# Kernel tuning notes

Hardware: AMD Instinct MI355X
Metric: run time of the kernel (lower is better)

## Reference

```python
import jax, jax.numpy as jnp
import numpy as np

TEMPERATURE = 0.2
EPS = 1e-12


def setup_inputs() -> dict:
    key = jax.random.key(0)
    k1, k2 = jax.random.split(key)
    x = jax.random.normal(k1, (16384, 2048), dtype=jnp.float32)
    protos = jax.random.normal(k2, (4096, 2048), dtype=jnp.float32)
    # buffer is initialized as row-normalized in the torch module
    protos = protos / jnp.maximum(jnp.linalg.norm(protos, axis=1, keepdims=True), EPS)
    return {"x": x, "prototypes": protos, "k": 16}


def reference(x, prototypes, k):
    # L2-normalize inputs (torch F.normalize uses eps clamp on the norm)
    xn = x / jnp.maximum(jnp.linalg.norm(x, axis=-1, keepdims=True), EPS)
    # cosine similarities: (B, P)
    sims = jnp.einsum("bd,pd->bp", xn, prototypes)
    topk_vals, topk_idx = jax.lax.top_k(sims, k)          # (B, k)
    topk_softmax = jax.nn.softmax(topk_vals / TEMPERATURE, axis=-1)
    rows = jnp.arange(sims.shape[0])[:, None]             # (B, 1)
    sparse_act = jnp.zeros_like(sims).at[rows, topk_idx].set(topk_softmax)
    return sparse_act
```

## Files before the change

### kernel.cpp

```cpp
#include <hip/hip_runtime.h>
#include <hip/hip_bf16.h>
#include <stdint.h>

typedef __attribute__((ext_vector_type(8))) short bf16x8;
typedef __attribute__((ext_vector_type(4))) float f32x4;
typedef unsigned short u16;

#define M_ROWS 16384
#define N_COLS 4096
#define K_DIM  2048
#define TOPK   16
#define KSEL   16
#define CAP    48
#define INV_T  5.0f
#define DELTA  0.05f

#define BM 128
#define BN 128
#define BK 64
#define NKT (K_DIM / BK)

__device__ __forceinline__ void async_cp16(const void* g, void* l) {
  __builtin_amdgcn_global_load_lds((const __attribute__((address_space(1))) uint32_t*)g,
                                   (__attribute__((address_space(3))) uint32_t*)l,
                                   16, 0, 0);
}

__device__ __forceinline__ u16 f2bf(float f) {
  __hip_bfloat16 h = __float2bfloat16(f);
  return *reinterpret_cast<u16*>(&h);
}
__device__ __forceinline__ float bf2f(u16 u) {
  return __uint_as_float(((uint32_t)u) << 16);
}
__device__ __forceinline__ uint2 pack4(float4 v) {
  uint2 r;
  r.x = (uint32_t)f2bf(v.x) | ((uint32_t)f2bf(v.y) << 16);
  r.y = (uint32_t)f2bf(v.z) | ((uint32_t)f2bf(v.w) << 16);
  return r;
}

__global__ __launch_bounds__(256) void prep_x_kernel(
    const float* __restrict__ x, u16* __restrict__ xh, float* __restrict__ invn) {
  const int row = blockIdx.x;
  const int t = threadIdx.x;
  const float4* xr = reinterpret_cast<const float4*>(x + (size_t)row * K_DIM);
  float4 v0 = xr[t];
  float4 v1 = xr[256 + t];
  float s = v0.x*v0.x + v0.y*v0.y + v0.z*v0.z + v0.w*v0.w
          + v1.x*v1.x + v1.y*v1.y + v1.z*v1.z + v1.w*v1.w;
  #pragma unroll
  for (int off = 1; off < 64; off <<= 1) s += __shfl_xor(s, off);
  __shared__ float ws4[4];
  if ((t & 63) == 0) ws4[t >> 6] = s;
  __syncthreads();
  if (t == 0) {
    float tot = ws4[0] + ws4[1] + ws4[2] + ws4[3];
    invn[row] = 1.0f / fmaxf(sqrtf(tot), 1e-12f);
  }
  uint2* xo = reinterpret_cast<uint2*>(xh + (size_t)row * K_DIM);
  xo[t] = pack4(v0);
  xo[256 + t] = pack4(v1);
}

__global__ __launch_bounds__(256) void prep_p_kernel(
    const float* __restrict__ p, u16* __restrict__ ph) {
  const int row = blockIdx.x;
  const int t = threadIdx.x;
  const float4* pr = reinterpret_cast<const float4*>(p + (size_t)row * K_DIM);
  uint2* po = reinterpret_cast<uint2*>(ph + (size_t)row * K_DIM);
  po[t] = pack4(pr[t]);
  po[256 + t] = pack4(pr[256 + t]);
}

__global__ __launch_bounds__(256) void gemm_bf16_kernel(
    const u16* __restrict__ A, const u16* __restrict__ B, u16* __restrict__ C) {
  __shared__ __align__(16) u16 sA[2][BM * BK];
  __shared__ __align__(16) u16 sB[2][BN * BK];
  const int t = threadIdx.x;
  const int lane = t & 63;
  const int wid = t >> 6;
  const int wm = wid >> 1, wn = wid & 1;
  const int tm0 = blockIdx.y * BM;
  const int tn0 = blockIdx.x * BN;
  const int lr = lane & 15;
  const int hi = lane >> 4;

  f32x4 acc[4][4];
  #pragma unroll
  for (int i = 0; i < 4; ++i)
    #pragma unroll
    for (int j = 0; j < 4; ++j)
      acc[i][j] = (f32x4){0.f, 0.f, 0.f, 0.f};

  int srow[4], soff[4];
  #pragma unroll
  for (int i = 0; i < 4; ++i) {
    int c = i * 256 + t;
    int r = c >> 3;
    int ib = (c & 7) << 4;
    srow[i] = r;
    soff[i] = ib ^ ((r & 7) << 4);
  }
  const char* Abase = (const char*)(A + (size_t)tm0 * K_DIM);
  const char* Bbase = (const char*)(B + (size_t)tn0 * K_DIM);

#define STAGE(slot, kt_) do {                                                 \
    const int kb_ = (kt_) * (BK * 2);                                         \
    _Pragma("unroll")                                                         \
    for (int i = 0; i < 4; ++i) {                                             \
      async_cp16(Abase + (size_t)srow[i] * (K_DIM * 2) + kb_ + soff[i],       \
                 (char*)sA[slot] + (i * 256 + t) * 16);                       \
      async_cp16(Bbase + (size_t)srow[i] * (K_DIM * 2) + kb_ + soff[i],       \
                 (char*)sB[slot] + (i * 256 + t) * 16);                       \
    }                                                                         \
  } while (0)

  STAGE(0, 0);
  STAGE(1, 1);

  for (int kt = 0; kt < NKT; ++kt) {
    if (kt + 1 < NKT) asm volatile("s_waitcnt vmcnt(8)" ::: "memory");
    else              asm volatile("s_waitcnt vmcnt(0)" ::: "memory");
    __builtin_amdgcn_sched_barrier(0);
    __builtin_amdgcn_s_barrier();
    asm volatile("" ::: "memory");

    const char* cA = (const char*)sA[kt & 1];
    const char* cB = (const char*)sB[kt & 1];
    bf16x8 af[4][2], bq[4][2];
    #pragma unroll
    for (int f = 0; f < 4; ++f) {
      #pragma unroll
      for (int kk = 0; kk < 2; ++kk) {
        int rowA = wm * 64 + f * 16 + lr;
        int inbA = (kk * 64 + (hi << 4)) ^ ((rowA & 7) << 4);
        af[f][kk] = *reinterpret_cast<const bf16x8*>(cA + rowA * 128 + inbA);
        int rowB = wn * 64 + f * 16 + lr;
        int inbB = (kk * 64 + (hi << 4)) ^ ((rowB & 7) << 4);
        bq[f][kk] = *reinterpret_cast<const bf16x8*>(cB + rowB * 128 + inbB);
      }
    }
    asm volatile("s_waitcnt lgkmcnt(0)" ::: "memory");
    __builtin_amdgcn_sched_barrier(0);
    if (kt + 2 < NKT) {
      __builtin_amdgcn_s_barrier();
      asm volatile("" ::: "memory");
      __builtin_amdgcn_sched_barrier(0);
      STAGE(kt & 1, kt + 2);
    }
    __builtin_amdgcn_s_setprio(1);
    #pragma unroll
    for (int kk = 0; kk < 2; ++kk)
      #pragma unroll
      for (int i = 0; i < 4; ++i)
        #pragma unroll
        for (int j = 0; j < 4; ++j)
          acc[i][j] = __builtin_amdgcn_mfma_f32_16x16x32_bf16(
              af[i][kk], bq[j][kk], acc[i][j], 0, 0, 0);
    __builtin_amdgcn_s_setprio(0);
  }
#undef STAGE

  #pragma unroll
  for (int i = 0; i < 4; ++i) {
    #pragma unroll
    for (int j = 0; j < 4; ++j) {
      int colg = tn0 + wn * 64 + j * 16 + lr;
      int rowb = tm0 + wm * 64 + i * 16 + (hi << 2);
      #pragma unroll
      for (int r = 0; r < 4; ++r) {
        __builtin_nontemporal_store(f2bf(acc[i][j][r]),
                                    &C[(size_t)(rowb + r) * N_COLS + colg]);
      }
    }
  }
}

__global__ __launch_bounds__(256) void topk_kernel(
    const float* __restrict__ x, const float* __restrict__ protos,
    const float* __restrict__ invn, const u16* __restrict__ sims,
    int* __restrict__ sposg, float* __restrict__ svalg) {
  const int row = blockIdx.x;
  const int t = threadIdx.x;
  const int lane = t & 63;
  const int wid = t >> 6;

  __shared__ __align__(16) f32x4 lx[512];
  __shared__ int hist[4][257];
  __shared__ int selInfo[2];
  __shared__ int   wtotC[4], wtotW[4];
  __shared__ int   cposC[16];
  __shared__ float cargC[16];
  __shared__ int   wpos[CAP];
  __shared__ float cexact[CAP];
  __shared__ int   spos[TOPK];
  __shared__ float sval[TOPK];

  const bf16x8* orow8 = reinterpret_cast<const bf16x8*>(sims + (size_t)row * N_COLS);
  float fv[16];
  uint32_t key[16];
  #pragma unroll
  for (int i = 0; i < 2; ++i) {
    bf16x8 v = __builtin_nontemporal_load(orow8 + i * 256 + t);
    #pragma unroll
    for (int c = 0; c < 8; ++c) {
      u16 u = (u16)v[c];
      fv[i * 8 + c] = bf2f(u);
      key[i * 8 + c] = (u & 0x8000) ? (uint32_t)(~u & 0xFFFF)
                                    : (uint32_t)(u | 0x8000);
    }
  }

  const f32x4* xr = reinterpret_cast<const f32x4*>(x + (size_t)row * K_DIM);
  lx[t] = __builtin_nontemporal_load(xr + t);
  lx[256 + t] = __builtin_nontemporal_load(xr + 256 + t);

  uint32_t T = 0;
  int K_rem = KSEL;
  #pragma unroll
  for (int pass = 0; pass < 2; ++pass) {
    const int shift = 8 - pass * 8;
    hist[0][t] = 0; hist[1][t] = 0; hist[2][t] = 0; hist[3][t] = 0;
    __syncthreads();
    #pragma unroll
    for (int j = 0; j < 16; ++j) {
      bool ok = (pass == 0) || ((key[j] >> 8) == T);
      if (ok) atomicAdd(&hist[wid][(key[j] >> shift) & 255], 1);
    }
    __syncthreads();
    if (wid == 0) {
      const int b0 = lane << 2;
      int h0 = hist[0][b0]     + hist[1][b0]     + hist[2][b0]     + hist[3][b0];
      int h1 = hist[0][b0 + 1] + hist[1][b0 + 1] + hist[2][b0 + 1] + hist[3][b0 + 1];
      int h2 = hist[0][b0 + 2] + hist[1][b0 + 2] + hist[2][b0 + 2] + hist[3][b0 + 2];
      int h3 = hist[0][b0 + 3] + hist[1][b0 + 3] + hist[2][b0 + 3] + hist[3][b0 + 3];
      int loc = h0 + h1 + h2 + h3;
      int s = loc;
      #pragma unroll
      for (int off = 1; off < 64; off <<= 1) {
        int o = __shfl_down(s, off);
        if (lane + off < 64) s += o;
      }
      const int tail = s - loc;
      int s3 = tail + h3;
      int s2 = s3 + h2;
      int s1 = s2 + h1;
      int s0 = s1 + h0;
      int ge[4] = {s0, s1, s2, s3};
      int hh[4] = {h0, h1, h2, h3};
      #pragma unroll
      for (int k = 0; k < 4; ++k) {
        int gt = ge[k] - hh[k];
        if (gt < K_rem && ge[k] >= K_rem) {
          selInfo[0] = b0 + k;
          selInfo[1] = K_rem - gt;
        }
      }
    }
    __syncthreads();
    T = (T << 8) | (uint32_t)selInfo[0];
    K_rem = selInfo[1];
  }
  const u16 ub = (T & 0x8000) ? (u16)(T ^ 0x8000) : (u16)(~T & 0xFFFF);
  const float a16 = bf2f(ub);
  const float vhi = a16 + DELTA;
  const float vlo = a16 - DELTA;
  const float inv = invn[row];

  int lcC = 0, lcW = 0;
  #pragma unroll
  for (int j = 0; j < 16; ++j) {
    float v = fv[j];
    if (v > vhi) ++lcC;
    else if (v >= vlo) ++lcW;
  }
  int pC = lcC, pW = lcW;
  #pragma unroll
  for (int off = 1; off < 64; off <<= 1) {
    int oC = __shfl_up(pC, off);
    int oW = __shfl_up(pW, off);
    if (lane >= off) { pC += oC; pW += oW; }
  }
  if (lane == 63) { wtotC[wid] = pC; wtotW[wid] = pW; }
  __syncthreads();
  int baseC = pC - lcC, baseW = pW - lcW;
  for (int w2 = 0; w2 < wid; ++w2) { baseC += wtotC[w2]; baseW += wtotW[w2]; }
  const int m  = wtotC[0] + wtotC[1] + wtotC[2] + wtotC[3];
  const int wc = min(wtotW[0] + wtotW[1] + wtotW[2] + wtotW[3], CAP);
  #pragma unroll
  for (int j = 0; j < 16; ++j) {
    float v = fv[j];
    int pos = (j >> 3) * 2048 + t * 8 + (j & 7);
    if (v > vhi) { cposC[baseC] = pos; cargC[baseC] = v; ++baseC; }
    else if (v >= vlo) { if (baseW < CAP) { wpos[baseW] = pos; ++baseW; } }
  }
  __syncthreads();

  for (int ci = wid; ci < wc; ci += 4) {
    int pidx = wpos[ci];
    const f32x4* pr = reinterpret_cast<const f32x4*>(protos + (size_t)pidx * K_DIM);
    float s = 0.f;
    #pragma unroll
    for (int i = 0; i < 8; ++i) {
      f32x4 pv = pr[i * 64 + lane];
      f32x4 xv = lx[i * 64 + lane];
      s = fmaf(pv.x, xv.x, s);
      s = fmaf(pv.y, xv.y, s);
      s = fmaf(pv.z, xv.z, s);
      s = fmaf(pv.w, xv.w, s);
    }
    #pragma unroll
    for (int off = 1; off < 64; off <<= 1) s += __shfl_xor(s, off);
    if (lane == 0) cexact[ci] = s * inv;
  }
  __syncthreads();

  if (wid == 0) {
    const int w_need = TOPK - m;
    float v = (lane < wc) ? cexact[lane] : -3.0e38f;
    int pos = (lane < wc) ? wpos[lane] : 0x7fffffff;
    int rank = 0;
    for (int j = 0; j < wc; ++j) {
      float vj = __shfl(v, j);
      int   pj = __shfl(pos, j);
      if (lane < wc && j != lane)
        if (vj > v || (vj == v && pj < pos)) rank++;
    }
    bool sel = (lane < wc) && (rank < w_need);
    unsigned long long bal = __ballot(sel);
    int slot = __popcll(bal & ((1ull << lane) - 1ull));
    if (sel) { spos[m + slot] = pos; sval[m + slot] = v; }
    if (lane < m) { spos[lane] = cposC[lane]; sval[lane] = cargC[lane] * inv; }
    float av = (lane < TOPK) ? sval[lane] : -3.0e38f;
    float vm = av;
    #pragma unroll
    for (int off = 1; off < 16; off <<= 1) vm = fmaxf(vm, __shfl_xor(vm, off));
    float e = (lane < TOPK) ? expf((av - vm) * INV_T) : 0.f;
    float se = e;
    #pragma unroll
    for (int off = 1; off < 16; off <<= 1) se += __shfl_xor(se, off);
    if (lane < TOPK) {
      sposg[(size_t)row * TOPK + lane] = spos[lane];
      svalg[(size_t)row * TOPK + lane] = e / se;
    }
  }
}

__global__ __launch_bounds__(256) void writer_kernel(
    const int* __restrict__ sposg, const float* __restrict__ svalg,
    float* __restrict__ out) {
  const int row = blockIdx.x;
  const int t = threadIdx.x;
  __shared__ int sp[TOPK];
  __shared__ float svv[TOPK];
  if (t < TOPK) {
    sp[t] = sposg[(size_t)row * TOPK + t];
    svv[t] = svalg[(size_t)row * TOPK + t];
  }
  __syncthreads();
  f32x4* orow4w = reinterpret_cast<f32x4*>(out + (size_t)row * N_COLS);
  #pragma unroll
  for (int i = 0; i < 4; ++i) {
    f32x4 o = (f32x4){0.f, 0.f, 0.f, 0.f};
    #pragma unroll
    for (int s = 0; s < TOPK; ++s) {
      int p = sp[s];
      if ((p >> 10) == i && ((p >> 2) & 255) == t) o[p & 3] = svv[s];
    }
    __builtin_nontemporal_store(o, orow4w + i * 256 + t);
  }
}

extern "C" void kernel_launch(void* const* d_in, const int* in_sizes, int n_in,
                              void* d_out, int out_size, void* d_ws, size_t ws_size,
                              hipStream_t stream) {
  const float* x = (const float*)d_in[0];
  const float* protos = (const float*)d_in[1];
  float* out = (float*)d_out;

  char* ws = (char*)d_ws;
  u16* xh = (u16*)ws;
  u16* ph = (u16*)(ws + (size_t)M_ROWS * K_DIM * 2);
  float* invn = (float*)(ws + (size_t)(M_ROWS + N_COLS) * K_DIM * 2);
  int*   sposg = (int*)(ws + (size_t)M_ROWS * K_DIM * 2);
  float* svalg = (float*)(ws + (size_t)M_ROWS * K_DIM * 2 + (size_t)M_ROWS * TOPK * 4);

  u16* simsbf = (u16*)d_out;

  prep_x_kernel<<<M_ROWS, 256, 0, stream>>>(x, xh, invn);
  prep_p_kernel<<<N_COLS, 256, 0, stream>>>(protos, ph);

  dim3 gg(N_COLS / BN, M_ROWS / BM);
  gemm_bf16_kernel<<<gg, 256, 0, stream>>>(xh, ph, simsbf);

  topk_kernel<<<M_ROWS, 256, 0, stream>>>(x, protos, invn, simsbf, sposg, svalg);
  writer_kernel<<<M_ROWS, 256, 0, stream>>>(sposg, svalg, out);
}
```

Baseline: 520.8 us.

## Enlarge GEMM tile to 256x128 with BK=32 and adjusted LDS swizzle

Doubles the M dimension of the bf16 GEMM block tile to 256 rows and halves the K step to 32, so each wave computes a 128x64 sub-tile with 32 accumulators. The LDS staging layout, XOR swizzle, per-thread load offsets and vmcnt wait count are reworked to match the new 64-byte rows. The aim is more MFMA work per byte loaded from global memory and shared memory. The cost is more accumulator registers, which may reduce occupancy, and twice as many K iterations with barriers. The grid launch must also shrink in y for the larger tile.

```diff
diff --git a/kernel.cpp b/kernel.cpp
--- a/kernel.cpp
+++ b/kernel.cpp
@@ -15,9 +15,9 @@
 #define INV_T  5.0f
 #define DELTA  0.05f
 
-#define BM 128
+#define BM 256
 #define BN 128
-#define BK 64
+#define BK 32
 #define NKT (K_DIM / BK)
 
 __device__ __forceinline__ void async_cp16(const void* g, void* l) {
@@ -86,21 +86,25 @@
   const int lr = lane & 15;
   const int hi = lane >> 4;
 
-  f32x4 acc[4][4];
-  #pragma unroll
-  for (int i = 0; i < 4; ++i)
+  f32x4 acc[8][4];
+  #pragma unroll
+  for (int i = 0; i < 8; ++i)
     #pragma unroll
     for (int j = 0; j < 4; ++j)
       acc[i][j] = (f32x4){0.f, 0.f, 0.f, 0.f};
 
-  int srow[4], soff[4];
-  #pragma unroll
-  for (int i = 0; i < 4; ++i) {
-    int c = i * 256 + t;
-    int r = c >> 3;
-    int ib = (c & 7) << 4;
-    srow[i] = r;
-    soff[i] = ib ^ ((r & 7) << 4);
+  int aoff[4], boff[2];
+  #pragma unroll
+  for (int c = 0; c < 4; ++c) {
+    int ci = c * 256 + t;
+    int r = ci >> 2;
+    aoff[c] = r * (K_DIM * 2) + (((ci & 3) ^ ((r >> 1) & 3)) << 4);
+  }
+  #pragma unroll
+  for (int c = 0; c < 2; ++c) {
+    int ci = c * 256 + t;
+    int r = ci >> 2;
+    boff[c] = r * (K_DIM * 2) + (((ci & 3) ^ ((r >> 1) & 3)) << 4);
   }
   const char* Abase = (const char*)(A + (size_t)tm0 * K_DIM);
   const char* Bbase = (const char*)(B + (size_t)tn0 * K_DIM);
@@ -108,19 +112,20 @@
 #define STAGE(slot, kt_) do {                                                 \
     const int kb_ = (kt_) * (BK * 2);                                         \
     _Pragma("unroll")                                                         \
-    for (int i = 0; i < 4; ++i) {                                             \
-      async_cp16(Abase + (size_t)srow[i] * (K_DIM * 2) + kb_ + soff[i],       \
-                 (char*)sA[slot] + (i * 256 + t) * 16);                       \
-      async_cp16(Bbase + (size_t)srow[i] * (K_DIM * 2) + kb_ + soff[i],       \
-                 (char*)sB[slot] + (i * 256 + t) * 16);                       \
-    }                                                                         \
+    for (int c = 0; c < 4; ++c)                                               \
+      async_cp16(Abase + aoff[c] + kb_,                                       \
+                 (char*)sA[slot] + (c * 256 + t) * 16);                       \
+    _Pragma("unroll")                                                         \
+    for (int c = 0; c < 2; ++c)                                               \
+      async_cp16(Bbase + boff[c] + kb_,                                       \
+                 (char*)sB[slot] + (c * 256 + t) * 16);                       \
   } while (0)
 
   STAGE(0, 0);
   STAGE(1, 1);
 
   for (int kt = 0; kt < NKT; ++kt) {
-    if (kt + 1 < NKT) asm volatile("s_waitcnt vmcnt(8)" ::: "memory");
+    if (kt + 1 < NKT) asm volatile("s_waitcnt vmcnt(6)" ::: "memory");
     else              asm volatile("s_waitcnt vmcnt(0)" ::: "memory");
     __builtin_amdgcn_sched_barrier(0);
     __builtin_amdgcn_s_barrier();
@@ -128,18 +133,18 @@
 
     const char* cA = (const char*)sA[kt & 1];
     const char* cB = (const char*)sB[kt & 1];
-    bf16x8 af[4][2], bq[4][2];
+    bf16x8 af[8], bq[4];
+    #pragma unroll
+    for (int f = 0; f < 8; ++f) {
+      int rA = wm * 128 + f * 16 + lr;
+      af[f] = *reinterpret_cast<const bf16x8*>(
+          cA + rA * 64 + ((hi ^ ((rA >> 1) & 3)) << 4));
+    }
     #pragma unroll
     for (int f = 0; f < 4; ++f) {
-      #pragma unroll
-      for (int kk = 0; kk < 2; ++kk) {
-        int rowA = wm * 64 + f * 16 + lr;
-        int inbA = (kk * 64 + (hi << 4)) ^ ((rowA & 7) << 4);
-        af[f][kk] = *reinterpret_cast<const bf16x8*>(cA + rowA * 128 + inbA);
-        int rowB = wn * 64 + f * 16 + lr;
-        int inbB = (kk * 64 + (hi << 4)) ^ ((rowB & 7) << 4);
-        bq[f][kk] = *reinterpret_cast<const bf16x8*>(cB + rowB * 128 + inbB);
-      }
+      int rB = wn * 64 + f * 16 + lr;
+      bq[f] = *reinterpret_cast<const bf16x8*>(
+          cB + rB * 64 + ((hi ^ ((rB >> 1) & 3)) << 4));
     }
     asm volatile("s_waitcnt lgkmcnt(0)" ::: "memory");
     __builtin_amdgcn_sched_barrier(0);
@@ -151,23 +156,21 @@
     }
     __builtin_amdgcn_s_setprio(1);
     #pragma unroll
-    for (int kk = 0; kk < 2; ++kk)
+    for (int i = 0; i < 8; ++i)
       #pragma unroll
-      for (int i = 0; i < 4; ++i)
-        #pragma unroll
-        for (int j = 0; j < 4; ++j)
-          acc[i][j] = __builtin_amdgcn_mfma_f32_16x16x32_bf16(
-              af[i][kk], bq[j][kk], acc[i][j], 0, 0, 0);
+      for (int j = 0; j < 4; ++j)
+        acc[i][j] = __builtin_amdgcn_mfma_f32_16x16x32_bf16(
+            af[i], bq[j], acc[i][j], 0, 0, 0);
     __builtin_amdgcn_s_setprio(0);
   }
 #undef STAGE
 
   #pragma unroll
-  for (int i = 0; i < 4; ++i) {
+  for (int i = 0; i < 8; ++i) {
     #pragma unroll
     for (int j = 0; j < 4; ++j) {
       int colg = tn0 + wn * 64 + j * 16 + lr;
-      int rowb = tm0 + wm * 64 + i * 16 + (hi << 2);
+      int rowb = tm0 + wm * 128 + i * 16 + (hi << 2);
       #pragma unroll
       for (int r = 0; r < 4; ++r) {
         __builtin_nontemporal_store(f2bf(acc[i][j][r]),
```

Measured after the change: 646.6 us. 24.2% more time.
